# Optimization experiments

Hardware: AMD Instinct MI355X
Metric: run time of the kernel (lower is better)

Reference implementation:

```python
import jax, jax.numpy as jnp
import numpy as np
import math

N_HEAD = 16

def setup_inputs() -> dict:
    key = jax.random.key(0)
    k1, k2, k3 = jax.random.split(key, 3)
    B, T, C = 4, 2048, 1024
    x = jax.random.normal(k1, (B, T, C), dtype=jnp.float32)
    W_attn = jax.random.normal(k2, (C, 3 * C), dtype=jnp.float32) * 0.02
    b_attn = jnp.zeros((3 * C,), dtype=jnp.float32)
    W_proj = jax.random.normal(k3, (C, C), dtype=jnp.float32) * 0.02
    b_proj = jnp.zeros((C,), dtype=jnp.float32)
    return {"x": x, "W_attn": W_attn, "b_attn": b_attn, "W_proj": W_proj, "b_proj": b_proj}

def reference(x, W_attn, b_attn, W_proj, b_proj):
    B, T, C = x.shape
    H = N_HEAD
    hd = C // H
    qkv = x @ W_attn + b_attn                      # [B,T,3C]
    # Faithful to source bug: q, k, v ALL built from the k-slice of qkv.
    k_slice = qkv[:, :, C:2 * C]
    k = k_slice.reshape(B, T, H, hd).transpose(0, 2, 1, 3)  # [B,H,T,hd]
    q = k
    v = k
    att = jnp.einsum('bhqd,bhkd->bhqk', q, k) / math.sqrt(hd)  # [B,H,T,T]
    causal = jnp.tril(jnp.ones((T, T), dtype=bool))
    att = jnp.where(causal[None, None], att, jnp.finfo(att.dtype).min)
    att = jax.nn.softmax(att, axis=-1)
    y = jnp.einsum('bhqk,bhkd->bhqd', att, v)      # [B,H,T,hd]
    y = y.transpose(0, 2, 1, 3).reshape(B, T, C)
    return y @ W_proj + b_proj
```

## Files before the change

### kernel.cpp

```cpp
#include <hip/hip_runtime.h>

#define T_SEQ 2048
#define C_DIM 1024
#define HD 64

typedef __attribute__((ext_vector_type(8))) short short8;
typedef __attribute__((ext_vector_type(4))) float f32x4;
typedef __attribute__((ext_vector_type(4))) unsigned int uint4v;

extern "C" __device__ float __ocml_native_exp2_f32(float);

__device__ __forceinline__ unsigned short f2bf(float f) {
  unsigned int u = __builtin_bit_cast(unsigned int, f);
  u += 0x7fffu + ((u >> 16) & 1u);
  return (unsigned short)(u >> 16);
}

__device__ __forceinline__ unsigned cvt_pk_bf16(float lo, float hi) {
  unsigned r;
  asm("v_cvt_pk_bf16_f32 %0, %1, %2" : "=v"(r) : "v"(lo), "v"(hi));
  return r;
}

__device__ __forceinline__ void gload_lds16(const void* g, void* l) {
  __builtin_amdgcn_global_load_lds(
      (const __attribute__((address_space(1))) void*)g,
      (__attribute__((address_space(3))) void*)l, 16, 0, 0);
}

__global__ __launch_bounds__(256) void transpose_w(
    const float* __restrict__ src, unsigned short* __restrict__ dst,
    int src_ld, int col_off) {
  __shared__ float tile[16][17];
  int n = blockIdx.x * 16 + threadIdx.x;
  int k = blockIdx.y * 16 + threadIdx.y;
  tile[threadIdx.y][threadIdx.x] = src[(size_t)k * src_ld + col_off + n];
  __syncthreads();
  int nn = blockIdx.x * 16 + threadIdx.y;
  int kk = blockIdx.y * 16 + threadIdx.x;
  dst[(size_t)nn * C_DIM + kk] = f2bf(tile[threadIdx.x][threadIdx.y]);
}

__global__ __launch_bounds__(256) void conv_x(
    const float* __restrict__ x, unsigned short* __restrict__ xb) {
  size_t idx = ((size_t)blockIdx.x * 256 + threadIdx.x) * 8;
  const f32x4* p = (const f32x4*)(x + idx);
  f32x4 a = p[0], b = p[1];
  short8 s;
#pragma unroll
  for (int i = 0; i < 4; ++i) {
    s[i]     = (short)f2bf(a[i]);
    s[i + 4] = (short)f2bf(b[i]);
  }
  *(short8*)(xb + idx) = s;
}

__global__ __launch_bounds__(256) void gemm_xw(
    const unsigned short* __restrict__ A, const unsigned short* __restrict__ Bt,
    const float* __restrict__ bias, unsigned short* __restrict__ out,
    unsigned short* __restrict__ vt) {
  __shared__ unsigned short Als[128 * 32];
  __shared__ unsigned short Bls[128 * 32];
  const int tid = threadIdx.x;
  const int l = tid & 63, w = tid >> 6;
  const int wr = w >> 1, wc = w & 1;
  const int rb = blockIdx.x * 128, cb = blockIdx.y * 128;
  const int brow = tid >> 2, bhalf = (tid & 3) * 8;
  f32x4 acc[4][4] = {};
  for (int kb = 0; kb < 1024; kb += 32) {
    gload_lds16(A + (size_t)(rb + brow) * 1024 + kb + bhalf,
                &Als[(size_t)w * 512]);
    gload_lds16(A + (size_t)(rb + 64 + brow) * 1024 + kb + bhalf,
                &Als[2048 + (size_t)w * 512]);
    gload_lds16(Bt + (size_t)(cb + brow) * 1024 + kb + bhalf,
                &Bls[(size_t)w * 512]);
    gload_lds16(Bt + (size_t)(cb + 64 + brow) * 1024 + kb + bhalf,
                &Bls[2048 + (size_t)w * 512]);
    __syncthreads();
    short8 af[4], bfr[4];
#pragma unroll
    for (int m = 0; m < 4; ++m)
      af[m] = *(const short8*)&Als[(wr * 64 + m * 16 + (l & 15)) * 32 + (l >> 4) * 8];
#pragma unroll
    for (int n = 0; n < 4; ++n)
      bfr[n] = *(const short8*)&Bls[(wc * 64 + n * 16 + (l & 15)) * 32 + (l >> 4) * 8];
#pragma unroll
    for (int m = 0; m < 4; ++m)
#pragma unroll
      for (int n = 0; n < 4; ++n)
        acc[m][n] = __builtin_amdgcn_mfma_f32_16x16x32_bf16(af[m], bfr[n], acc[m][n], 0, 0, 0);
    __syncthreads();
  }
  const int rg = (l >> 4) * 4, cg = l & 15;
#pragma unroll
  for (int m = 0; m < 4; ++m)
#pragma unroll
    for (int n = 0; n < 4; ++n) {
      int col = cb + wc * 64 + n * 16 + cg;
      float bv = bias[col];
      int row0 = rb + wr * 64 + m * 16 + rg;
      unsigned short e0 = f2bf(acc[m][n][0] + bv);
      unsigned short e1 = f2bf(acc[m][n][1] + bv);
      unsigned short e2 = f2bf(acc[m][n][2] + bv);
      unsigned short e3 = f2bf(acc[m][n][3] + bv);
      size_t bhd = (size_t)((row0 >> 11) * 16 + (col >> 6));
      size_t kidx = (bhd * T_SEQ + (row0 & 2047)) * HD + (col & 63);
      out[kidx]          = e0;
      out[kidx + HD]     = e1;
      out[kidx + 2 * HD] = e2;
      out[kidx + 3 * HD] = e3;
      unsigned long long pv = (unsigned long long)e0 | ((unsigned long long)e1 << 16)
                            | ((unsigned long long)e2 << 32) | ((unsigned long long)e3 << 48);
      *(unsigned long long*)&vt[(bhd * HD + (col & 63)) * T_SEQ + (row0 & 2047)] = pv;
    }
}

__global__ __launch_bounds__(256) void gemm_yw(
    const unsigned short* __restrict__ A, const unsigned short* __restrict__ Bt,
    const float* __restrict__ bias, float* __restrict__ out) {
  __shared__ unsigned short Als[128 * 32];
  __shared__ unsigned short Bls[128 * 32];
  const int tid = threadIdx.x;
  const int l = tid & 63, w = tid >> 6;
  const int wr = w >> 1, wc = w & 1;
  const int rb = blockIdx.x * 128, cb = blockIdx.y * 128;
  const int brow = tid >> 2, bhalf = (tid & 3) * 8;
  f32x4 acc[4][4] = {};
  for (int kb = 0; kb < 1024; kb += 32) {
    gload_lds16(A + (size_t)(rb + brow) * 1024 + kb + bhalf,
                &Als[(size_t)w * 512]);
    gload_lds16(A + (size_t)(rb + 64 + brow) * 1024 + kb + bhalf,
                &Als[2048 + (size_t)w * 512]);
    gload_lds16(Bt + (size_t)(cb + brow) * 1024 + kb + bhalf,
                &Bls[(size_t)w * 512]);
    gload_lds16(Bt + (size_t)(cb + 64 + brow) * 1024 + kb + bhalf,
                &Bls[2048 + (size_t)w * 512]);
    __syncthreads();
    short8 af[4], bfr[4];
#pragma unroll
    for (int m = 0; m < 4; ++m)
      af[m] = *(const short8*)&Als[(wr * 64 + m * 16 + (l & 15)) * 32 + (l >> 4) * 8];
#pragma unroll
    for (int n = 0; n < 4; ++n)
      bfr[n] = *(const short8*)&Bls[(wc * 64 + n * 16 + (l & 15)) * 32 + (l >> 4) * 8];
#pragma unroll
    for (int m = 0; m < 4; ++m)
#pragma unroll
      for (int n = 0; n < 4; ++n)
        acc[m][n] = __builtin_amdgcn_mfma_f32_16x16x32_bf16(af[m], bfr[n], acc[m][n], 0, 0, 0);
    __syncthreads();
  }
  const int rg = (l >> 4) * 4, cg = l & 15;
#pragma unroll
  for (int m = 0; m < 4; ++m)
#pragma unroll
    for (int n = 0; n < 4; ++n) {
      int col = cb + wc * 64 + n * 16 + cg;
      float bv = bias[col];
#pragma unroll
      for (int r = 0; r < 4; ++r) {
        int row = rb + wr * 64 + m * 16 + rg + r;
        out[(size_t)row * 1024 + col] = acc[m][n][r] + bv;
      }
    }
}

__device__ __forceinline__ void sm_group(
    f32x4 (&s)[4], int qq, int kvb, bool needmask, int g,
    float& mrun, float& lrun, f32x4 (&yacc)[4],
    int src01, int src23, bool hi2, short8 (&pa)[2]) {
  if (needmask) {
    const int lim = qq - kvb;
#pragma unroll
    for (int b = 0; b < 4; ++b)
#pragma unroll
      for (int r = 0; r < 4; ++r)
        if (16 * b + 4 * g + r > lim) s[b][r] = -INFINITY;
  }
  float mt = fmaxf(fmaxf(s[0][0], s[0][1]), fmaxf(s[0][2], s[0][3]));
#pragma unroll
  for (int b = 1; b < 4; ++b)
    mt = fmaxf(mt, fmaxf(fmaxf(s[b][0], s[b][1]), fmaxf(s[b][2], s[b][3])));
  mt = fmaxf(mt, __shfl_xor(mt, 16));
  mt = fmaxf(mt, __shfl_xor(mt, 32));
  if (!__all(mt <= mrun + 11.5416f)) {
    float mn = fmaxf(mrun, mt);
    float al = __ocml_native_exp2_f32(mrun - mn);
    mrun = mn;
    lrun *= al;
    float a0 = __shfl(al, 4 * g + 0);
    float a1 = __shfl(al, 4 * g + 1);
    float a2 = __shfl(al, 4 * g + 2);
    float a3 = __shfl(al, 4 * g + 3);
#pragma unroll
    for (int nb = 0; nb < 4; ++nb) {
      yacc[nb][0] *= a0; yacc[nb][1] *= a1;
      yacc[nb][2] *= a2; yacc[nb][3] *= a3;
    }
  }
  float ps = 0.f;
  unsigned pk[4][2];
#pragma unroll
  for (int b = 0; b < 4; ++b) {
    float p0 = __ocml_native_exp2_f32(s[b][0] - mrun);
    float p1 = __ocml_native_exp2_f32(s[b][1] - mrun);
    float p2 = __ocml_native_exp2_f32(s[b][2] - mrun);
    float p3 = __ocml_native_exp2_f32(s[b][3] - mrun);
    ps += (p0 + p1) + (p2 + p3);
    pk[b][0] = cvt_pk_bf16(p0, p1);
    pk[b][1] = cvt_pk_bf16(p2, p3);
  }
  ps += __shfl_xor(ps, 16);
  ps += __shfl_xor(ps, 32);
  lrun += ps;
  {
    unsigned x0a = (unsigned)__shfl((int)pk[0][0], src01);
    unsigned x1a = (unsigned)__shfl((int)pk[1][0], src01);
    unsigned x0b = (unsigned)__shfl((int)pk[0][1], src01);
    unsigned x1b = (unsigned)__shfl((int)pk[1][1], src01);
    unsigned y0a = (unsigned)__shfl((int)pk[0][0], src23);
    unsigned y1a = (unsigned)__shfl((int)pk[1][0], src23);
    unsigned y0b = (unsigned)__shfl((int)pk[0][1], src23);
    unsigned y1b = (unsigned)__shfl((int)pk[1][1], src23);
    uint4v u;
    u.x = hi2 ? x1a : x0a;
    u.y = hi2 ? x1b : x0b;
    u.z = hi2 ? y1a : y0a;
    u.w = hi2 ? y1b : y0b;
    pa[0] = __builtin_bit_cast(short8, u);
  }
  {
    unsigned x0a = (unsigned)__shfl((int)pk[2][0], src01);
    unsigned x1a = (unsigned)__shfl((int)pk[3][0], src01);
    unsigned x0b = (unsigned)__shfl((int)pk[2][1], src01);
    unsigned x1b = (unsigned)__shfl((int)pk[3][1], src01);
    unsigned y0a = (unsigned)__shfl((int)pk[2][0], src23);
    unsigned y1a = (unsigned)__shfl((int)pk[3][0], src23);
    unsigned y0b = (unsigned)__shfl((int)pk[2][1], src23);
    unsigned y1b = (unsigned)__shfl((int)pk[3][1], src23);
    uint4v u;
    u.x = hi2 ? x1a : x0a;
    u.y = hi2 ? x1b : x0b;
    u.z = hi2 ? y1a : y0a;
    u.w = hi2 ? y1b : y0b;
    pa[1] = __builtin_bit_cast(short8, u);
  }
}

__global__ __launch_bounds__(128, 4) void attn_fwd(
    const unsigned short* __restrict__ Khb, const unsigned short* __restrict__ Vt,
    unsigned short* __restrict__ Y) {
  const int id = blockIdx.x;
  const int xcd = id & 7;
  const int r8  = id >> 3;
  const int bh  = xcd * 8 + (r8 & 7);
  const int chunk = 63 - (r8 >> 3);
  const int tid = threadIdx.x;
  const int w = tid >> 6;
  const int l = tid & 63;
  const int i = l & 15, g = l >> 4;
  const unsigned short* kbase = Khb + (size_t)bh * T_SEQ * HD;
  const unsigned short* vbase = Vt + (size_t)bh * HD * T_SEQ;

  const int q0 = chunk * 32;
  const int qA = q0 + i, qB = q0 + 16 + i;
  const int nt = (q0 + 31) / 64 + 1;
  const int half = (nt + 1) >> 1;
  const int tBeg = w ? half : 0;
  const int tEnd = w ? nt : half;

  __shared__ float Ylds[32][68];
  __shared__ float Mlds[32];
  __shared__ float Llds[32];

  short8 qa0 = *(const short8*)(kbase + (size_t)qA * HD + g * 8);
  short8 qa1 = *(const short8*)(kbase + (size_t)qA * HD + 32 + g * 8);
  short8 qb0 = *(const short8*)(kbase + (size_t)qB * HD + g * 8);
  short8 qb1 = *(const short8*)(kbase + (size_t)qB * HD + 32 + g * 8);

  f32x4 ya[4] = {}, yb[4] = {};
  float mA = -INFINITY, lA = 0.f, mB = -INFINITY, lB = 0.f;

  const int src01 = i + ((g & 1) << 5);
  const int src23 = src01 + 16;
  const bool hi2 = (g >> 1) != 0;
  const float SCL = 0.18033688f;

  for (int t = tBeg; t < tEnd; ++t) {
    const int kvb = t * 64;
    f32x4 sa[4], sb[4];
#pragma unroll
    for (int b = 0; b < 4; ++b) {
      const unsigned short* kp = kbase + (size_t)(kvb + 16 * b + i) * HD + g * 8;
      short8 k0 = *(const short8*)kp;
      short8 k1 = *(const short8*)(kp + 32);
      f32x4 acc = {};
      acc = __builtin_amdgcn_mfma_f32_16x16x32_bf16(k0, qa0, acc, 0, 0, 0);
      acc = __builtin_amdgcn_mfma_f32_16x16x32_bf16(k1, qa1, acc, 0, 0, 0);
      sa[b] = acc;
      f32x4 acc2 = {};
      acc2 = __builtin_amdgcn_mfma_f32_16x16x32_bf16(k0, qb0, acc2, 0, 0, 0);
      acc2 = __builtin_amdgcn_mfma_f32_16x16x32_bf16(k1, qb1, acc2, 0, 0, 0);
      sb[b] = acc2;
    }
#pragma unroll
    for (int b = 0; b < 4; ++b)
#pragma unroll
      for (int r = 0; r < 4; ++r) { sa[b][r] *= SCL; sb[b][r] *= SCL; }

    const bool needmask = (kvb + 63 > q0);
    short8 paA[2], paB[2];
    sm_group(sa, qA, kvb, needmask, g, mA, lA, ya, src01, src23, hi2, paA);
    sm_group(sb, qB, kvb, needmask, g, mB, lB, yb, src01, src23, hi2, paB);

#pragma unroll
    for (int c = 0; c < 2; ++c)
#pragma unroll
      for (int nb = 0; nb < 4; ++nb) {
        short8 vf = *(const short8*)(vbase + (size_t)(nb * 16 + i) * T_SEQ + kvb + c * 32 + g * 8);
        ya[nb] = __builtin_amdgcn_mfma_f32_16x16x32_bf16(paA[c], vf, ya[nb], 0, 0, 0);
        yb[nb] = __builtin_amdgcn_mfma_f32_16x16x32_bf16(paB[c], vf, yb[nb], 0, 0, 0);
      }
  }

  if (w == 1) {
#pragma unroll
    for (int nb = 0; nb < 4; ++nb)
#pragma unroll
      for (int r = 0; r < 4; ++r) {
        Ylds[4 * g + r][nb * 16 + i]      = ya[nb][r];
        Ylds[16 + 4 * g + r][nb * 16 + i] = yb[nb][r];
      }
    if (l < 16) {
      Mlds[l]      = mA;
      Llds[l]      = lA;
      Mlds[16 + l] = mB;
      Llds[16 + l] = lB;
    }
  }
  __syncthreads();
  if (w == 0) {
    const int bb = bh >> 4, hh = bh & 15;
    size_t rowA = ((size_t)bb * T_SEQ + q0 + 4 * g) * C_DIM;
#pragma unroll
    for (int r = 0; r < 4; ++r) {
      float m0 = __shfl(mA, 4 * g + r);
      float l0 = __shfl(lA, 4 * g + r);
      float m1 = Mlds[4 * g + r];
      float l1 = Llds[4 * g + r];
      float mm = fmaxf(m0, m1);
      float e0 = __ocml_native_exp2_f32(m0 - mm);
      float e1 = __ocml_native_exp2_f32(m1 - mm);
      float inv = 1.f / (l0 * e0 + l1 * e1);
      float w0 = e0 * inv, w1 = e1 * inv;
#pragma unroll
      for (int nb = 0; nb < 4; ++nb) {
        int col = hh * 64 + nb * 16 + i;
        Y[rowA + (size_t)r * C_DIM + col] =
            f2bf(ya[nb][r] * w0 + Ylds[4 * g + r][nb * 16 + i] * w1);
      }
    }
    size_t rowB = rowA + (size_t)16 * C_DIM;
#pragma unroll
    for (int r = 0; r < 4; ++r) {
      float m0 = __shfl(mB, 4 * g + r);
      float l0 = __shfl(lB, 4 * g + r);
      float m1 = Mlds[16 + 4 * g + r];
      float l1 = Llds[16 + 4 * g + r];
      float mm = fmaxf(m0, m1);
      float e0 = __ocml_native_exp2_f32(m0 - mm);
      float e1 = __ocml_native_exp2_f32(m1 - mm);
      float inv = 1.f / (l0 * e0 + l1 * e1);
      float w0 = e0 * inv, w1 = e1 * inv;
#pragma unroll
      for (int nb = 0; nb < 4; ++nb) {
        int col = hh * 64 + nb * 16 + i;
        Y[rowB + (size_t)r * C_DIM + col] =
            f2bf(yb[nb][r] * w0 + Ylds[16 + 4 * g + r][nb * 16 + i] * w1);
      }
    }
  }
}

extern "C" void kernel_launch(void* const* d_in, const int* in_sizes, int n_in,
                              void* d_out, int out_size, void* d_ws, size_t ws_size,
                              hipStream_t stream) {
  const float* x      = (const float*)d_in[0];
  const float* W_attn = (const float*)d_in[1];
  const float* b_attn = (const float*)d_in[2];
  const float* W_proj = (const float*)d_in[3];
  const float* b_proj = (const float*)d_in[4];
  float* out = (float*)d_out;

  unsigned short* Wkt  = (unsigned short*)d_ws;
  unsigned short* Wpt  = Wkt + (size_t)1024 * 1024;
  unsigned short* Khb  = Wpt + (size_t)1024 * 1024;
  unsigned short* Ybuf = Khb + (size_t)8192 * 1024;
  unsigned short* Vtb  = Ybuf + (size_t)8192 * 1024;
  unsigned short* xb   = Ybuf;

  transpose_w<<<dim3(64, 64), dim3(16, 16), 0, stream>>>(W_attn, Wkt, 3072, 1024);
  transpose_w<<<dim3(64, 64), dim3(16, 16), 0, stream>>>(W_proj, Wpt, 1024, 0);

  conv_x<<<dim3(4096), 256, 0, stream>>>(x, xb);

  gemm_xw<<<dim3(64, 8), 256, 0, stream>>>(xb, Wkt, b_attn + 1024, Khb, Vtb);

  attn_fwd<<<dim3(4096), 128, 0, stream>>>(Khb, Vtb, Ybuf);

  gemm_yw<<<dim3(64, 8), 256, 0, stream>>>(Ybuf, Wpt, b_proj, out);
}
```

Measured before the change: 204.2 us.

## Rewrite attention with single-wave 32x32 MFMA tiles and no split-KV merge

The attention kernel now runs one 64-lane wave per 32-query block and uses 32x32x16 bf16 MFMAs over 32-key tiles, replacing the two-wave split-KV design built on 16x16x32 MFMAs. This removes the LDS merge of the two partial softmax states and the __syncthreads, and cuts the shuffle traffic needed to reshape P for the PV product. It also drops the XCD-aware block-to-head remapping. In exchange, each block has half the threads and walks every KV tile serially, which may lower per-block parallelism and L2 locality.

```diff
diff --git a/kernel.cpp b/kernel.cpp
--- a/kernel.cpp
+++ b/kernel.cpp
@@ -6,6 +6,7 @@
 
 typedef __attribute__((ext_vector_type(8))) short short8;
 typedef __attribute__((ext_vector_type(4))) float f32x4;
+typedef __attribute__((ext_vector_type(16))) float f32x16;
 typedef __attribute__((ext_vector_type(4))) unsigned int uint4v;
 
 extern "C" __device__ float __ocml_native_exp2_f32(float);
@@ -165,220 +166,117 @@
     }
 }
 
-__device__ __forceinline__ void sm_group(
-    f32x4 (&s)[4], int qq, int kvb, bool needmask, int g,
-    float& mrun, float& lrun, f32x4 (&yacc)[4],
-    int src01, int src23, bool hi2, short8 (&pa)[2]) {
-  if (needmask) {
-    const int lim = qq - kvb;
-#pragma unroll
-    for (int b = 0; b < 4; ++b)
-#pragma unroll
-      for (int r = 0; r < 4; ++r)
-        if (16 * b + 4 * g + r > lim) s[b][r] = -INFINITY;
-  }
-  float mt = fmaxf(fmaxf(s[0][0], s[0][1]), fmaxf(s[0][2], s[0][3]));
-#pragma unroll
-  for (int b = 1; b < 4; ++b)
-    mt = fmaxf(mt, fmaxf(fmaxf(s[b][0], s[b][1]), fmaxf(s[b][2], s[b][3])));
-  mt = fmaxf(mt, __shfl_xor(mt, 16));
-  mt = fmaxf(mt, __shfl_xor(mt, 32));
-  if (!__all(mt <= mrun + 11.5416f)) {
-    float mn = fmaxf(mrun, mt);
-    float al = __ocml_native_exp2_f32(mrun - mn);
-    mrun = mn;
-    lrun *= al;
-    float a0 = __shfl(al, 4 * g + 0);
-    float a1 = __shfl(al, 4 * g + 1);
-    float a2 = __shfl(al, 4 * g + 2);
-    float a3 = __shfl(al, 4 * g + 3);
-#pragma unroll
-    for (int nb = 0; nb < 4; ++nb) {
-      yacc[nb][0] *= a0; yacc[nb][1] *= a1;
-      yacc[nb][2] *= a2; yacc[nb][3] *= a3;
-    }
-  }
-  float ps = 0.f;
-  unsigned pk[4][2];
-#pragma unroll
-  for (int b = 0; b < 4; ++b) {
-    float p0 = __ocml_native_exp2_f32(s[b][0] - mrun);
-    float p1 = __ocml_native_exp2_f32(s[b][1] - mrun);
-    float p2 = __ocml_native_exp2_f32(s[b][2] - mrun);
-    float p3 = __ocml_native_exp2_f32(s[b][3] - mrun);
-    ps += (p0 + p1) + (p2 + p3);
-    pk[b][0] = cvt_pk_bf16(p0, p1);
-    pk[b][1] = cvt_pk_bf16(p2, p3);
-  }
-  ps += __shfl_xor(ps, 16);
-  ps += __shfl_xor(ps, 32);
-  lrun += ps;
-  {
-    unsigned x0a = (unsigned)__shfl((int)pk[0][0], src01);
-    unsigned x1a = (unsigned)__shfl((int)pk[1][0], src01);
-    unsigned x0b = (unsigned)__shfl((int)pk[0][1], src01);
-    unsigned x1b = (unsigned)__shfl((int)pk[1][1], src01);
-    unsigned y0a = (unsigned)__shfl((int)pk[0][0], src23);
-    unsigned y1a = (unsigned)__shfl((int)pk[1][0], src23);
-    unsigned y0b = (unsigned)__shfl((int)pk[0][1], src23);
-    unsigned y1b = (unsigned)__shfl((int)pk[1][1], src23);
-    uint4v u;
-    u.x = hi2 ? x1a : x0a;
-    u.y = hi2 ? x1b : x0b;
-    u.z = hi2 ? y1a : y0a;
-    u.w = hi2 ? y1b : y0b;
-    pa[0] = __builtin_bit_cast(short8, u);
-  }
-  {
-    unsigned x0a = (unsigned)__shfl((int)pk[2][0], src01);
-    unsigned x1a = (unsigned)__shfl((int)pk[3][0], src01);
-    unsigned x0b = (unsigned)__shfl((int)pk[2][1], src01);
-    unsigned x1b = (unsigned)__shfl((int)pk[3][1], src01);
-    unsigned y0a = (unsigned)__shfl((int)pk[2][0], src23);
-    unsigned y1a = (unsigned)__shfl((int)pk[3][0], src23);
-    unsigned y0b = (unsigned)__shfl((int)pk[2][1], src23);
-    unsigned y1b = (unsigned)__shfl((int)pk[3][1], src23);
-    uint4v u;
-    u.x = hi2 ? x1a : x0a;
-    u.y = hi2 ? x1b : x0b;
-    u.z = hi2 ? y1a : y0a;
-    u.w = hi2 ? y1b : y0b;
-    pa[1] = __builtin_bit_cast(short8, u);
-  }
-}
-
-__global__ __launch_bounds__(128, 4) void attn_fwd(
+__global__ __launch_bounds__(64, 4) void attn_fwd(
     const unsigned short* __restrict__ Khb, const unsigned short* __restrict__ Vt,
     unsigned short* __restrict__ Y) {
   const int id = blockIdx.x;
-  const int xcd = id & 7;
-  const int r8  = id >> 3;
-  const int bh  = xcd * 8 + (r8 & 7);
-  const int chunk = 63 - (r8 >> 3);
-  const int tid = threadIdx.x;
-  const int w = tid >> 6;
-  const int l = tid & 63;
-  const int i = l & 15, g = l >> 4;
+  const int bh = id & 63;
+  const int chunk = 63 - (id >> 6);
+  const int l = threadIdx.x & 63;
+  const int q31 = l & 31;
+  const int h = l >> 5;
   const unsigned short* kbase = Khb + (size_t)bh * T_SEQ * HD;
   const unsigned short* vbase = Vt + (size_t)bh * HD * T_SEQ;
 
   const int q0 = chunk * 32;
-  const int qA = q0 + i, qB = q0 + 16 + i;
-  const int nt = (q0 + 31) / 64 + 1;
-  const int half = (nt + 1) >> 1;
-  const int tBeg = w ? half : 0;
-  const int tEnd = w ? nt : half;
-
-  __shared__ float Ylds[32][68];
-  __shared__ float Mlds[32];
-  __shared__ float Llds[32];
-
-  short8 qa0 = *(const short8*)(kbase + (size_t)qA * HD + g * 8);
-  short8 qa1 = *(const short8*)(kbase + (size_t)qA * HD + 32 + g * 8);
-  short8 qb0 = *(const short8*)(kbase + (size_t)qB * HD + g * 8);
-  short8 qb1 = *(const short8*)(kbase + (size_t)qB * HD + 32 + g * 8);
-
-  f32x4 ya[4] = {}, yb[4] = {};
-  float mA = -INFINITY, lA = 0.f, mB = -INFINITY, lB = 0.f;
-
-  const int src01 = i + ((g & 1) << 5);
-  const int src23 = src01 + 16;
-  const bool hi2 = (g >> 1) != 0;
+  const int qme = q0 + q31;
+  const int nt = chunk + 1;
+
+  short8 qf[4];
+#pragma unroll
+  for (int c = 0; c < 4; ++c)
+    qf[c] = *(const short8*)(kbase + (size_t)(q0 + q31) * HD + 16 * c + 8 * h);
+
+  f32x16 y0 = {}, y1 = {};
+  float m = -INFINITY, lsum = 0.f;
   const float SCL = 0.18033688f;
 
-  for (int t = tBeg; t < tEnd; ++t) {
-    const int kvb = t * 64;
-    f32x4 sa[4], sb[4];
-#pragma unroll
-    for (int b = 0; b < 4; ++b) {
-      const unsigned short* kp = kbase + (size_t)(kvb + 16 * b + i) * HD + g * 8;
-      short8 k0 = *(const short8*)kp;
-      short8 k1 = *(const short8*)(kp + 32);
-      f32x4 acc = {};
-      acc = __builtin_amdgcn_mfma_f32_16x16x32_bf16(k0, qa0, acc, 0, 0, 0);
-      acc = __builtin_amdgcn_mfma_f32_16x16x32_bf16(k1, qa1, acc, 0, 0, 0);
-      sa[b] = acc;
-      f32x4 acc2 = {};
-      acc2 = __builtin_amdgcn_mfma_f32_16x16x32_bf16(k0, qb0, acc2, 0, 0, 0);
-      acc2 = __builtin_amdgcn_mfma_f32_16x16x32_bf16(k1, qb1, acc2, 0, 0, 0);
-      sb[b] = acc2;
-    }
-#pragma unroll
-    for (int b = 0; b < 4; ++b)
-#pragma unroll
-      for (int r = 0; r < 4; ++r) { sa[b][r] *= SCL; sb[b][r] *= SCL; }
-
-    const bool needmask = (kvb + 63 > q0);
-    short8 paA[2], paB[2];
-    sm_group(sa, qA, kvb, needmask, g, mA, lA, ya, src01, src23, hi2, paA);
-    sm_group(sb, qB, kvb, needmask, g, mB, lB, yb, src01, src23, hi2, paB);
-
-#pragma unroll
-    for (int c = 0; c < 2; ++c)
-#pragma unroll
-      for (int nb = 0; nb < 4; ++nb) {
-        short8 vf = *(const short8*)(vbase + (size_t)(nb * 16 + i) * T_SEQ + kvb + c * 32 + g * 8);
-        ya[nb] = __builtin_amdgcn_mfma_f32_16x16x32_bf16(paA[c], vf, ya[nb], 0, 0, 0);
-        yb[nb] = __builtin_amdgcn_mfma_f32_16x16x32_bf16(paB[c], vf, yb[nb], 0, 0, 0);
+  for (int t = 0; t < nt; ++t) {
+    const int kvb = t * 32;
+    f32x16 st = {};
+#pragma unroll
+    for (int c = 0; c < 4; ++c) {
+      short8 kf = *(const short8*)(kbase + (size_t)(kvb + q31) * HD + 16 * c + 8 * h);
+      st = __builtin_amdgcn_mfma_f32_32x32x16_bf16(kf, qf[c], st, 0, 0, 0);
+    }
+    const bool needmask = (kvb + 31 > q0);
+    if (needmask) {
+#pragma unroll
+      for (int r = 0; r < 16; ++r) {
+        int koff = (r & 3) + 8 * (r >> 2) + 4 * h;
+        if (kvb + koff > qme) st[r] = -INFINITY;
       }
-  }
-
-  if (w == 1) {
-#pragma unroll
-    for (int nb = 0; nb < 4; ++nb)
-#pragma unroll
-      for (int r = 0; r < 4; ++r) {
-        Ylds[4 * g + r][nb * 16 + i]      = ya[nb][r];
-        Ylds[16 + 4 * g + r][nb * 16 + i] = yb[nb][r];
+    }
+#pragma unroll
+    for (int r = 0; r < 16; ++r) st[r] *= SCL;
+    float mt = st[0];
+#pragma unroll
+    for (int r = 1; r < 16; ++r) mt = fmaxf(mt, st[r]);
+    mt = fmaxf(mt, __shfl_xor(mt, 32));
+    if (!__all(mt <= m + 11.5416f)) {
+      float mn = fmaxf(m, mt);
+      float al = __ocml_native_exp2_f32(m - mn);
+      m = mn;
+      lsum *= al;
+#pragma unroll
+      for (int r = 0; r < 16; ++r) {
+        int qrow = (r & 3) + 8 * (r >> 2) + 4 * h;
+        float ar = __shfl(al, qrow);
+        y0[r] *= ar;
+        y1[r] *= ar;
       }
-    if (l < 16) {
-      Mlds[l]      = mA;
-      Llds[l]      = lA;
-      Mlds[16 + l] = mB;
-      Llds[16 + l] = lB;
-    }
-  }
-  __syncthreads();
-  if (w == 0) {
-    const int bb = bh >> 4, hh = bh & 15;
-    size_t rowA = ((size_t)bb * T_SEQ + q0 + 4 * g) * C_DIM;
-#pragma unroll
-    for (int r = 0; r < 4; ++r) {
-      float m0 = __shfl(mA, 4 * g + r);
-      float l0 = __shfl(lA, 4 * g + r);
-      float m1 = Mlds[4 * g + r];
-      float l1 = Llds[4 * g + r];
-      float mm = fmaxf(m0, m1);
-      float e0 = __ocml_native_exp2_f32(m0 - mm);
-      float e1 = __ocml_native_exp2_f32(m1 - mm);
-      float inv = 1.f / (l0 * e0 + l1 * e1);
-      float w0 = e0 * inv, w1 = e1 * inv;
-#pragma unroll
-      for (int nb = 0; nb < 4; ++nb) {
-        int col = hh * 64 + nb * 16 + i;
-        Y[rowA + (size_t)r * C_DIM + col] =
-            f2bf(ya[nb][r] * w0 + Ylds[4 * g + r][nb * 16 + i] * w1);
-      }
-    }
-    size_t rowB = rowA + (size_t)16 * C_DIM;
-#pragma unroll
-    for (int r = 0; r < 4; ++r) {
-      float m0 = __shfl(mB, 4 * g + r);
-      float l0 = __shfl(lB, 4 * g + r);
-      float m1 = Mlds[16 + 4 * g + r];
-      float l1 = Llds[16 + 4 * g + r];
-      float mm = fmaxf(m0, m1);
-      float e0 = __ocml_native_exp2_f32(m0 - mm);
-      float e1 = __ocml_native_exp2_f32(m1 - mm);
-      float inv = 1.f / (l0 * e0 + l1 * e1);
-      float w0 = e0 * inv, w1 = e1 * inv;
-#pragma unroll
-      for (int nb = 0; nb < 4; ++nb) {
-        int col = hh * 64 + nb * 16 + i;
-        Y[rowB + (size_t)r * C_DIM + col] =
-            f2bf(yb[nb][r] * w0 + Ylds[16 + 4 * g + r][nb * 16 + i] * w1);
-      }
-    }
+    }
+    float p[16];
+    float ps = 0.f;
+#pragma unroll
+    for (int r = 0; r < 16; ++r) {
+      p[r] = __ocml_native_exp2_f32(st[r] - m);
+      ps += p[r];
+    }
+    lsum += ps;
+    unsigned pk[8];
+#pragma unroll
+    for (int u = 0; u < 8; ++u) pk[u] = cvt_pk_bf16(p[2 * u], p[2 * u + 1]);
+    {
+      unsigned s1 = (unsigned)__shfl_xor((int)(h ? pk[0] : pk[2]), 32);
+      unsigned s2 = (unsigned)__shfl_xor((int)(h ? pk[1] : pk[3]), 32);
+      uint4v u;
+      u.x = h ? s1 : pk[0];
+      u.y = h ? s2 : pk[1];
+      u.z = h ? pk[2] : s1;
+      u.w = h ? pk[3] : s2;
+      short8 paf = __builtin_bit_cast(short8, u);
+      short8 vf0 = *(const short8*)(vbase + (size_t)q31 * T_SEQ + kvb + 8 * h);
+      short8 vf1 = *(const short8*)(vbase + (size_t)(32 + q31) * T_SEQ + kvb + 8 * h);
+      y0 = __builtin_amdgcn_mfma_f32_32x32x16_bf16(paf, vf0, y0, 0, 0, 0);
+      y1 = __builtin_amdgcn_mfma_f32_32x32x16_bf16(paf, vf1, y1, 0, 0, 0);
+    }
+    {
+      unsigned s1 = (unsigned)__shfl_xor((int)(h ? pk[4] : pk[6]), 32);
+      unsigned s2 = (unsigned)__shfl_xor((int)(h ? pk[5] : pk[7]), 32);
+      uint4v u;
+      u.x = h ? s1 : pk[4];
+      u.y = h ? s2 : pk[5];
+      u.z = h ? pk[6] : s1;
+      u.w = h ? pk[7] : s2;
+      short8 paf = __builtin_bit_cast(short8, u);
+      short8 vf0 = *(const short8*)(vbase + (size_t)q31 * T_SEQ + kvb + 16 + 8 * h);
+      short8 vf1 = *(const short8*)(vbase + (size_t)(32 + q31) * T_SEQ + kvb + 16 + 8 * h);
+      y0 = __builtin_amdgcn_mfma_f32_32x32x16_bf16(paf, vf0, y0, 0, 0, 0);
+      y1 = __builtin_amdgcn_mfma_f32_32x32x16_bf16(paf, vf1, y1, 0, 0, 0);
+    }
+  }
+
+  lsum += __shfl_xor(lsum, 32);
+  float linv = 1.f / lsum;
+  const int bb = bh >> 4, hh = bh & 15;
+#pragma unroll
+  for (int r = 0; r < 16; ++r) {
+    int qrow = (r & 3) + 8 * (r >> 2) + 4 * h;
+    float lv = __shfl(linv, qrow);
+    size_t row = ((size_t)bb * T_SEQ + q0 + qrow) * C_DIM + hh * 64;
+    Y[row + q31]      = f2bf(y0[r] * lv);
+    Y[row + 32 + q31] = f2bf(y1[r] * lv);
   }
 }
 
@@ -406,7 +304,7 @@
 
   gemm_xw<<<dim3(64, 8), 256, 0, stream>>>(xb, Wkt, b_attn + 1024, Khb, Vtb);
 
-  attn_fwd<<<dim3(4096), 128, 0, stream>>>(Khb, Vtb, Ybuf);
+  attn_fwd<<<dim3(4096), 64, 0, stream>>>(Khb, Vtb, Ybuf);
 
   gemm_yw<<<dim3(64, 8), 256, 0, stream>>>(Ybuf, Wpt, b_proj, out);
 }
```

New measurement: 207.1 us. No clear change (+1.4%).
